# Performance work log

Hardware: AMD Instinct MI355X
Metric: run time of the kernel (lower is better)

Reference implementation:

```python
import jax, jax.numpy as jnp
import numpy as np

DECAY = 0.99
EPS = 1e-05
DIM = 512
N_EMBED = 4096
B, H, W = 32, 32, 32


def setup_inputs() -> dict:
    key = jax.random.key(0)
    k1, k2, k3, k4, k5 = jax.random.split(key, 5)
    inp = jax.random.normal(k1, (B, H, W, DIM), dtype=jnp.float32)
    labels = jax.random.randint(k2, (B * H * W,), 0, N_EMBED)
    embed = jax.random.normal(k3, (DIM, N_EMBED), dtype=jnp.float32)
    cluster_size = jax.random.uniform(k4, (N_EMBED,), dtype=jnp.float32)
    embed_avg = jax.random.normal(k5, (DIM, N_EMBED), dtype=jnp.float32)
    return {"input": inp, "labels": labels, "embed": embed,
            "cluster_size": cluster_size, "embed_avg": embed_avg}


def reference(input, labels, embed, cluster_size, embed_avg):
    dim, n_embed = embed.shape
    flatten = input.reshape(-1, dim)                      # [N, dim]

    # codebook gather (F.embedding on embed.T)
    embed_ind = labels.reshape(input.shape[:-1])          # [B, H, W]
    quantize = jnp.take(embed.T, embed_ind, axis=0)       # [B, H, W, dim]

    # training EMA update: onehot-scatter expressed as segment_sum
    # (math identical to flatten.T @ one_hot(labels))
    onehot_sum = jnp.zeros((n_embed,), flatten.dtype).at[labels].add(1.0)   # [n_embed]
    embed_sum = jax.ops.segment_sum(flatten, labels, num_segments=n_embed).T  # [dim, n_embed]

    new_cluster_size = cluster_size * DECAY + (1.0 - DECAY) * onehot_sum
    new_embed_avg = embed_avg * DECAY + (1.0 - DECAY) * embed_sum
    n = new_cluster_size.sum()
    cs = (new_cluster_size + EPS) / (n + n_embed * EPS) * n
    new_embed = new_embed_avg / cs[None, :]

    diff = jnp.mean((jax.lax.stop_gradient(quantize) - input) ** 2)
    return (quantize, diff, embed_ind, new_embed, new_cluster_size, new_embed_avg)
```

## Files before the change

### kernel.cpp

```cpp
#include <hip/hip_runtime.h>

#define DIMV   512
#define NEMB   4096
#define NTOK   32768
#define TOTAL  (NTOK * DIMV)

#define OFF_Q    0u
#define OFF_DIFF 16777216u
#define OFF_IND  16777217u
#define OFF_NE   16809985u
#define OFF_NCS  18907137u
#define OFF_NEA  18911233u

#define WS_SUMT    0u
#define WS_BINCNT  2097152u
#define WS_BINST   2101248u
#define WS_CURSOR  2105344u
#define WS_SORTED  2109440u
#define WS_DIFF    2142208u
#define WS_NSUM    2142209u

#define DECAYF 0.99f
#define OMDF   0.01f
#define EPSF   1e-5f

__global__ void k_hist(const int* __restrict__ labels,
                       float* __restrict__ out,
                       int* __restrict__ bin_count) {
    int n = blockIdx.x * 256 + threadIdx.x;
    int lab = labels[n];
    out[OFF_IND + n] = (float)lab;
    atomicAdd(&bin_count[lab], 1);
}

__global__ void k_zero(int* __restrict__ bin_count, float* __restrict__ diff_acc) {
    int i = blockIdx.x * 256 + threadIdx.x;
    bin_count[i] = 0;
    if (i == 0) diff_acc[0] = 0.f;
}

__global__ void k_scan(const int* __restrict__ bin_count,
                       const float* __restrict__ cluster_size,
                       int* __restrict__ bin_start,
                       int* __restrict__ cursor,
                       float* __restrict__ out,
                       float* __restrict__ n_sum) {
    __shared__ int   part[256];
    __shared__ float fred[256];
    int t = threadIdx.x;
    int base = t * 16;
    int loc[16];
    int s = 0; float nl = 0.f;
    #pragma unroll
    for (int i = 0; i < 16; ++i) {
        int cc = bin_count[base + i];
        loc[i] = s; s += cc;
        float ncs = cluster_size[base + i] * DECAYF + OMDF * (float)cc;
        out[OFF_NCS + base + i] = ncs;
        nl += ncs;
    }
    part[t] = s;
    fred[t] = nl;
    __syncthreads();
    for (int o = 1; o < 256; o <<= 1) {
        int v = (t >= o) ? part[t - o] : 0;
        __syncthreads();
        part[t] += v;
        __syncthreads();
    }
    for (int o = 128; o > 0; o >>= 1) {
        if (t < o) fred[t] += fred[t + o];
        __syncthreads();
    }
    if (t == 0) n_sum[0] = fred[0];
    int off = (t == 0) ? 0 : part[t - 1];
    #pragma unroll
    for (int i = 0; i < 16; ++i) {
        bin_start[base + i] = off + loc[i];
        cursor[base + i]    = off + loc[i];
    }
}

__global__ void k_scatter(const int* __restrict__ labels,
                          int* __restrict__ cursor,
                          int* __restrict__ sorted_tok) {
    int n = blockIdx.x * 256 + threadIdx.x;
    int lab = labels[n];
    int pos = atomicAdd(&cursor[lab], 1);
    sorted_tok[pos] = n;
}

__global__ __launch_bounds__(256) void k_perlabel(
        const float* __restrict__ inp,
        const float* __restrict__ embed,
        const int*   __restrict__ sorted_tok,
        const int*   __restrict__ bin_start,
        const int*   __restrict__ bin_count,
        float* __restrict__ out,
        float* __restrict__ sumT,
        float* __restrict__ diff_acc) {
    int t    = threadIdx.x;
    int wave = t >> 6;
    int lane = t & 63;
    int e    = (blockIdx.x << 2) | wave;
    int d0   = lane << 3;

    const float* col = embed + e;
    float4 qa, qb;
    qa.x = col[(size_t)(d0 + 0) * NEMB];
    qa.y = col[(size_t)(d0 + 1) * NEMB];
    qa.z = col[(size_t)(d0 + 2) * NEMB];
    qa.w = col[(size_t)(d0 + 3) * NEMB];
    qb.x = col[(size_t)(d0 + 4) * NEMB];
    qb.y = col[(size_t)(d0 + 5) * NEMB];
    qb.z = col[(size_t)(d0 + 6) * NEMB];
    qb.w = col[(size_t)(d0 + 7) * NEMB];

    int start = bin_start[e];
    int cnt   = bin_count[e];

    float4 sa = make_float4(0, 0, 0, 0);
    float4 sb = make_float4(0, 0, 0, 0);
    float dacc = 0.f;

    for (int base = 0; base < cnt; base += 64) {
        int m = min(64, cnt - base);
        int idx = (lane < m) ? sorted_tok[start + base + lane] : 0;
        for (int sub = 0; sub < m; sub += 8) {
            int mm = min(8, m - sub);
            int n[8];
            float4 xa[8], xb[8];
            #pragma unroll
            for (int j = 0; j < 8; ++j) {
                if (j < mm) {
                    n[j] = __shfl(idx, sub + j);
                    const float4* r =
                        (const float4*)(inp + (size_t)n[j] * DIMV + d0);
                    xa[j] = r[0];
                    xb[j] = r[1];
                }
            }
            #pragma unroll
            for (int j = 0; j < 8; ++j) {
                if (j < mm) {
                    sa.x += xa[j].x; sa.y += xa[j].y;
                    sa.z += xa[j].z; sa.w += xa[j].w;
                    sb.x += xb[j].x; sb.y += xb[j].y;
                    sb.z += xb[j].z; sb.w += xb[j].w;
                    float t0 = qa.x - xa[j].x, t1 = qa.y - xa[j].y;
                    float t2 = qa.z - xa[j].z, t3 = qa.w - xa[j].w;
                    float u0 = qb.x - xb[j].x, u1 = qb.y - xb[j].y;
                    float u2 = qb.z - xb[j].z, u3 = qb.w - xb[j].w;
                    dacc += t0 * t0 + t1 * t1 + t2 * t2 + t3 * t3
                          + u0 * u0 + u1 * u1 + u2 * u2 + u3 * u3;
                    float4* orow =
                        (float4*)(out + OFF_Q + (size_t)n[j] * DIMV + d0);
                    orow[0] = qa;
                    orow[1] = qb;
                }
            }
        }
    }

    float* so = sumT + (size_t)e * DIMV + d0;
    *(float4*)(so)     = sa;
    *(float4*)(so + 4) = sb;

    for (int o = 32; o > 0; o >>= 1) dacc += __shfl_down(dacc, o);
    if (lane == 0) atomicAdd(diff_acc, dacc);
}

__global__ __launch_bounds__(256) void k_trans_final(
        const float* __restrict__ embed_avg,
        const float* __restrict__ sumT,
        const float* __restrict__ n_sum,
        const float* __restrict__ diff_acc,
        float* __restrict__ out) {
    __shared__ float tile[32][33];
    int tx = threadIdx.x & 31;
    int ty = threadIdx.x >> 5;
    int e0 = (blockIdx.x & 127) << 5;
    int d0 = (blockIdx.x >> 7) << 5;
    for (int i = 0; i < 4; ++i) {
        int er = ty + i * 8;
        tile[er][tx] = sumT[(size_t)(e0 + er) * DIMV + d0 + tx];
    }
    __syncthreads();
    float nsum = n_sum[0];
    float ncs  = out[OFF_NCS + e0 + tx];
    float cs   = (ncs + EPSF) / (nsum + (float)NEMB * EPSF) * nsum;
    float inv  = 1.0f / cs;
    for (int i = 0; i < 4; ++i) {
        int dr = d0 + ty + i * 8;
        size_t o = (size_t)dr * NEMB + e0 + tx;
        float val = DECAYF * embed_avg[o] + OMDF * tile[tx][ty + i * 8];
        out[OFF_NEA + o] = val;
        out[OFF_NE + o]  = val * inv;
    }
    if (blockIdx.x == 0 && threadIdx.x == 0)
        out[OFF_DIFF] = diff_acc[0] * (1.0f / (float)TOTAL);
}

extern "C" void kernel_launch(void* const* d_in, const int* in_sizes, int n_in,
                              void* d_out, int out_size, void* d_ws, size_t ws_size,
                              hipStream_t stream) {
    const float* inp          = (const float*)d_in[0];
    const int*   labels       = (const int*)  d_in[1];
    const float* embed        = (const float*)d_in[2];
    const float* cluster_size = (const float*)d_in[3];
    const float* embed_avg    = (const float*)d_in[4];
    float* out = (float*)d_out;

    float* wsf        = (float*)d_ws;
    float* sumT       = wsf + WS_SUMT;
    int*   bin_count  = (int*)(wsf + WS_BINCNT);
    int*   bin_start  = (int*)(wsf + WS_BINST);
    int*   cursor     = (int*)(wsf + WS_CURSOR);
    int*   sorted_tok = (int*)(wsf + WS_SORTED);
    float* diff_acc   = wsf + WS_DIFF;
    float* n_sum      = wsf + WS_NSUM;

    k_zero      <<<16,   256, 0, stream>>>(bin_count, diff_acc);
    k_hist      <<<128,  256, 0, stream>>>(labels, out, bin_count);
    k_scan      <<<1,    256, 0, stream>>>(bin_count, cluster_size, bin_start,
                                           cursor, out, n_sum);
    k_scatter   <<<128,  256, 0, stream>>>(labels, cursor, sorted_tok);
    k_perlabel  <<<1024, 256, 0, stream>>>(inp, embed, sorted_tok, bin_start,
                                           bin_count, out, sumT, diff_acc);
    k_trans_final<<<2048,256, 0, stream>>>(embed_avg, sumT, n_sum, diff_acc, out);
}
```

Before: 226.7 us.

## Assign one codeword per block with four waves splitting the dimension

The per-label kernel now gives each codeword a whole 256-thread block, with each wave covering 128 dimensions using float2 loads, instead of one wave per codeword with float4x2 loads. This gives four times as many blocks and more parallelism per label, and it cuts the per-thread register footprint. The cost is narrower memory accesses and more blocks reading the same token index list. Separately, the zeroing kernel is replaced by hipMemsetAsync, and the diff accumulator is now reset inside the scan kernel.

```diff
diff --git a/kernel.cpp b/kernel.cpp
--- a/kernel.cpp
+++ b/kernel.cpp
@@ -33,18 +33,13 @@
     atomicAdd(&bin_count[lab], 1);
 }
 
-__global__ void k_zero(int* __restrict__ bin_count, float* __restrict__ diff_acc) {
-    int i = blockIdx.x * 256 + threadIdx.x;
-    bin_count[i] = 0;
-    if (i == 0) diff_acc[0] = 0.f;
-}
-
 __global__ void k_scan(const int* __restrict__ bin_count,
                        const float* __restrict__ cluster_size,
                        int* __restrict__ bin_start,
                        int* __restrict__ cursor,
                        float* __restrict__ out,
-                       float* __restrict__ n_sum) {
+                       float* __restrict__ n_sum,
+                       float* __restrict__ diff_acc) {
     __shared__ int   part[256];
     __shared__ float fred[256];
     int t = threadIdx.x;
@@ -72,7 +67,7 @@
         if (t < o) fred[t] += fred[t + o];
         __syncthreads();
     }
-    if (t == 0) n_sum[0] = fred[0];
+    if (t == 0) { n_sum[0] = fred[0]; diff_acc[0] = 0.f; }
     int off = (t == 0) ? 0 : part[t - 1];
     #pragma unroll
     for (int i = 0; i < 16; ++i) {
@@ -100,27 +95,19 @@
         float* __restrict__ sumT,
         float* __restrict__ diff_acc) {
     int t    = threadIdx.x;
-    int wave = t >> 6;
+    int g    = t >> 6;
     int lane = t & 63;
-    int e    = (blockIdx.x << 2) | wave;
-    int d0   = lane << 3;
-
-    const float* col = embed + e;
-    float4 qa, qb;
-    qa.x = col[(size_t)(d0 + 0) * NEMB];
-    qa.y = col[(size_t)(d0 + 1) * NEMB];
-    qa.z = col[(size_t)(d0 + 2) * NEMB];
-    qa.w = col[(size_t)(d0 + 3) * NEMB];
-    qb.x = col[(size_t)(d0 + 4) * NEMB];
-    qb.y = col[(size_t)(d0 + 5) * NEMB];
-    qb.z = col[(size_t)(d0 + 6) * NEMB];
-    qb.w = col[(size_t)(d0 + 7) * NEMB];
+    int e    = blockIdx.x;
+    int d0   = (g << 7) | (lane << 1);
+
+    float2 q;
+    q.x = embed[(size_t)(d0 + 0) * NEMB + e];
+    q.y = embed[(size_t)(d0 + 1) * NEMB + e];
 
     int start = bin_start[e];
     int cnt   = bin_count[e];
 
-    float4 sa = make_float4(0, 0, 0, 0);
-    float4 sb = make_float4(0, 0, 0, 0);
+    float2 s2 = make_float2(0.f, 0.f);
     float dacc = 0.f;
 
     for (int base = 0; base < cnt; base += 64) {
@@ -129,42 +116,27 @@
         for (int sub = 0; sub < m; sub += 8) {
             int mm = min(8, m - sub);
             int n[8];
-            float4 xa[8], xb[8];
+            float2 x[8];
             #pragma unroll
             for (int j = 0; j < 8; ++j) {
                 if (j < mm) {
                     n[j] = __shfl(idx, sub + j);
-                    const float4* r =
-                        (const float4*)(inp + (size_t)n[j] * DIMV + d0);
-                    xa[j] = r[0];
-                    xb[j] = r[1];
+                    x[j] = *(const float2*)(inp + (size_t)n[j] * DIMV + d0);
                 }
             }
             #pragma unroll
             for (int j = 0; j < 8; ++j) {
                 if (j < mm) {
-                    sa.x += xa[j].x; sa.y += xa[j].y;
-                    sa.z += xa[j].z; sa.w += xa[j].w;
-                    sb.x += xb[j].x; sb.y += xb[j].y;
-                    sb.z += xb[j].z; sb.w += xb[j].w;
-                    float t0 = qa.x - xa[j].x, t1 = qa.y - xa[j].y;
-                    float t2 = qa.z - xa[j].z, t3 = qa.w - xa[j].w;
-                    float u0 = qb.x - xb[j].x, u1 = qb.y - xb[j].y;
-                    float u2 = qb.z - xb[j].z, u3 = qb.w - xb[j].w;
-                    dacc += t0 * t0 + t1 * t1 + t2 * t2 + t3 * t3
-                          + u0 * u0 + u1 * u1 + u2 * u2 + u3 * u3;
-                    float4* orow =
-                        (float4*)(out + OFF_Q + (size_t)n[j] * DIMV + d0);
-                    orow[0] = qa;
-                    orow[1] = qb;
+                    s2.x += x[j].x; s2.y += x[j].y;
+                    float t0 = q.x - x[j].x, t1 = q.y - x[j].y;
+                    dacc += t0 * t0 + t1 * t1;
+                    *(float2*)(out + OFF_Q + (size_t)n[j] * DIMV + d0) = q;
                 }
             }
         }
     }
 
-    float* so = sumT + (size_t)e * DIMV + d0;
-    *(float4*)(so)     = sa;
-    *(float4*)(so + 4) = sb;
+    *(float2*)(sumT + (size_t)e * DIMV + d0) = s2;
 
     for (int o = 32; o > 0; o >>= 1) dacc += __shfl_down(dacc, o);
     if (lane == 0) atomicAdd(diff_acc, dacc);
@@ -220,12 +192,12 @@
     float* diff_acc   = wsf + WS_DIFF;
     float* n_sum      = wsf + WS_NSUM;
 
-    k_zero      <<<16,   256, 0, stream>>>(bin_count, diff_acc);
+    hipMemsetAsync(bin_count, 0, NEMB * sizeof(int), stream);
     k_hist      <<<128,  256, 0, stream>>>(labels, out, bin_count);
     k_scan      <<<1,    256, 0, stream>>>(bin_count, cluster_size, bin_start,
-                                           cursor, out, n_sum);
+                                           cursor, out, n_sum, diff_acc);
     k_scatter   <<<128,  256, 0, stream>>>(labels, cursor, sorted_tok);
-    k_perlabel  <<<1024, 256, 0, stream>>>(inp, embed, sorted_tok, bin_start,
+    k_perlabel  <<<4096, 256, 0, stream>>>(inp, embed, sorted_tok, bin_start,
                                            bin_count, out, sumT, diff_acc);
     k_trans_final<<<2048,256, 0, stream>>>(embed_avg, sumT, n_sum, diff_acc, out);
 }
```

New measurement: 364.4 us. 1.61x slower.
